# Optimization experiments

Hardware: AMD Instinct MI355X
Metric: run time of the kernel (lower is better)

The kernel has to match this reference:

```python
import jax, jax.numpy as jnp
import numpy as np

EMBED_DIM = 2048
NUM_HEADS = 16
HEAD_DIM = EMBED_DIM // NUM_HEADS
SEQ_LEN = 2048
ROPE_BASE = 10000.0


def rope_cache(seq_len, dim, base=ROPE_BASE):
    inv_freq = 1.0 / (base ** (jnp.arange(0, dim, 2, dtype=jnp.float32) / dim))
    t = jnp.arange(seq_len, dtype=jnp.float32)
    freqs = jnp.einsum('s,d->sd', t, inv_freq)  # [S, D/2]
    return jnp.cos(freqs), jnp.sin(freqs)


def apply_rope_interleaved(x, cos, sin):
    # x: [B, S, H, D]; interleaved pairs (even, odd)
    B, S, H, D = x.shape
    xp = x.reshape(B, S, H, D // 2, 2)
    x1, x2 = xp[..., 0], xp[..., 1]
    c = cos[None, :, None, :]
    s = sin[None, :, None, :]
    o1 = x1 * c - x2 * s
    o2 = x1 * s + x2 * c
    return jnp.stack([o1, o2], axis=-1).reshape(B, S, H, D)


def setup_inputs() -> dict:
    key = jax.random.key(0)
    ks = jax.random.split(key, 5)
    B = 2
    scale = 0.02
    x = jax.random.normal(ks[0], (B, SEQ_LEN, EMBED_DIM), dtype=jnp.float32)
    Wq = jax.random.normal(ks[1], (EMBED_DIM, EMBED_DIM), dtype=jnp.float32) * scale
    Wk = jax.random.normal(ks[2], (EMBED_DIM, EMBED_DIM), dtype=jnp.float32) * scale
    Wv = jax.random.normal(ks[3], (EMBED_DIM, EMBED_DIM), dtype=jnp.float32) * scale
    Wo = jax.random.normal(ks[4], (EMBED_DIM, EMBED_DIM), dtype=jnp.float32) * scale
    return {"x": x, "Wq": Wq, "Wk": Wk, "Wv": Wv, "Wo": Wo}


def reference(x, Wq, Wk, Wv, Wo):
    B, S, E = x.shape
    H, D = NUM_HEADS, HEAD_DIM
    # projections (nn.Linear: y = x @ W.T; here W stored as [out, in])
    q = (x @ Wq.T).reshape(B, S, H, D)
    k = (x @ Wk.T).reshape(B, S, H, D)
    v = (x @ Wv.T).reshape(B, S, H, D)
    cos, sin = rope_cache(S, D)
    q = apply_rope_interleaved(q, cos, sin)
    k = apply_rope_interleaved(k, cos, sin)
    # causal attention, flash-attn semantics: scale = head_dim**-0.5, fp32 softmax
    scale = 1.0 / jnp.sqrt(jnp.float32(D))
    scores = jnp.einsum('bqhd,bkhd->bhqk', q, k) * scale
    causal = jnp.tril(jnp.ones((S, S), dtype=bool))
    scores = jnp.where(causal[None, None], scores, jnp.float32(-jnp.inf))
    probs = jax.nn.softmax(scores.astype(jnp.float32), axis=-1)
    attn = jnp.einsum('bhqk,bkhd->bqhd', probs.astype(v.dtype), v)
    attn = attn.reshape(B, S, H * D)
    return attn @ Wo.T
```

## Files before the change

kernel.cpp:

```cpp
#include <hip/hip_runtime.h>
#include <cstdint>
#include <cmath>

typedef short s16x8 __attribute__((ext_vector_type(8)));
typedef float f32x4 __attribute__((ext_vector_type(4)));
typedef int   i32x4 __attribute__((ext_vector_type(4)));
typedef unsigned short u16;

#define E_DIM 2048
#define SEQ   2048
#define NB    2
#define NH    16
#define HD    128
#define BS_TOT 4096

__device__ __forceinline__ u16 f2bf(float f) {
  unsigned u = __float_as_uint(f);
  u += 0x7fffu + ((u >> 16) & 1u);
  return (u16)(u >> 16);
}
__device__ __forceinline__ float bf2f(u16 h) {
  return __uint_as_float(((unsigned)h) << 16);
}
__device__ __forceinline__ float rmax16(float v) {
  v = fmaxf(v, __shfl_xor(v, 1));
  v = fmaxf(v, __shfl_xor(v, 2));
  v = fmaxf(v, __shfl_xor(v, 4));
  v = fmaxf(v, __shfl_xor(v, 8));
  return v;
}
__device__ __forceinline__ float rsum16(float v) {
  v += __shfl_xor(v, 1);
  v += __shfl_xor(v, 2);
  v += __shfl_xor(v, 4);
  v += __shfl_xor(v, 8);
  return v;
}

__device__ __forceinline__ void gll16(const u16* g, u16* l) {
  __builtin_amdgcn_global_load_lds(
      (const __attribute__((address_space(1))) void*)g,
      (__attribute__((address_space(3))) void*)l, 16, 0, 0);
}

__global__ __launch_bounds__(256) void cast_kernel(const float* __restrict__ in,
                                                   u16* __restrict__ out) {
  const size_t t = (size_t)blockIdx.x * 256 + threadIdx.x;
  const float* p = in + t * 8;
  f32x4 a = *(const f32x4*)p;
  f32x4 b = *(const f32x4*)(p + 4);
  union { u16 u[8]; i32x4 v; } r;
  r.u[0] = f2bf(a[0]); r.u[1] = f2bf(a[1]); r.u[2] = f2bf(a[2]); r.u[3] = f2bf(a[3]);
  r.u[4] = f2bf(b[0]); r.u[5] = f2bf(b[1]); r.u[6] = f2bf(b[2]); r.u[7] = f2bf(b[3]);
  *(i32x4*)(out + t * 8) = r.v;
}

template <typename OT, bool CVTA>
__global__ __launch_bounds__(256) void gemm_nt(const void* __restrict__ Av,
                                               const u16* __restrict__ B,
                                               OT* __restrict__ C,
                                               int M, int N, int K) {
  __shared__ __align__(16) u16 As[128 * 64];
  __shared__ __align__(16) u16 Bs[128 * 64];
  const int t  = threadIdx.x;
  const int w  = t >> 6, l = t & 63, lq = l >> 4, lm = l & 15;
  const int wr = w >> 1, wc = w & 1;
  const int m0 = blockIdx.y * 128, n0 = blockIdx.x * 128;

  const f32x4 fzero = {0.f, 0.f, 0.f, 0.f};
  f32x4 acc[4][4];
#pragma unroll
  for (int mi = 0; mi < 4; ++mi)
#pragma unroll
    for (int ni = 0; ni < 4; ++ni) acc[mi][ni] = fzero;

  for (int k0 = 0; k0 < K; k0 += 64) {
    __syncthreads();
    if constexpr (CVTA) {
      const float* A = (const float*)Av;
#pragma unroll
      for (int i = 0; i < 4; ++i) {
        const int ci = i * 256 + t;
        const int r = ci >> 3, c = ci & 7, gq = c ^ (r & 7);
        const float* s = A + (size_t)(m0 + r) * K + k0 + gq * 8;
        f32x4 a = *(const f32x4*)s;
        f32x4 b = *(const f32x4*)(s + 4);
        union { u16 u[8]; i32x4 v; } rr;
        rr.u[0] = f2bf(a[0]); rr.u[1] = f2bf(a[1]); rr.u[2] = f2bf(a[2]); rr.u[3] = f2bf(a[3]);
        rr.u[4] = f2bf(b[0]); rr.u[5] = f2bf(b[1]); rr.u[6] = f2bf(b[2]); rr.u[7] = f2bf(b[3]);
        *(i32x4*)(As + ci * 8) = rr.v;
      }
    } else {
      const u16* A = (const u16*)Av;
#pragma unroll
      for (int i = 0; i < 4; ++i) {
        const int ci = i * 256 + t;
        const int r = ci >> 3, c = ci & 7, gq = c ^ (r & 7);
        gll16(A + (size_t)(m0 + r) * K + k0 + gq * 8, As + ci * 8);
      }
    }
#pragma unroll
    for (int i = 0; i < 4; ++i) {
      const int ci = i * 256 + t;
      const int r = ci >> 3, c = ci & 7, gq = c ^ (r & 7);
      gll16(B + (size_t)(n0 + r) * K + k0 + gq * 8, Bs + ci * 8);
    }
    __syncthreads();
#pragma unroll
    for (int ks = 0; ks < 2; ++ks) {
      s16x8 af[4], bf[4];
#pragma unroll
      for (int mi = 0; mi < 4; ++mi) {
        const int ra = wr * 64 + mi * 16 + lm;
        af[mi] = *(const s16x8*)(As + ra * 64 + (((ks * 4 + lq) ^ (ra & 7)) << 3));
      }
#pragma unroll
      for (int ni = 0; ni < 4; ++ni) {
        const int rb = wc * 64 + ni * 16 + lm;
        bf[ni] = *(const s16x8*)(Bs + rb * 64 + (((ks * 4 + lq) ^ (rb & 7)) << 3));
      }
#pragma unroll
      for (int mi = 0; mi < 4; ++mi)
#pragma unroll
        for (int ni = 0; ni < 4; ++ni)
          acc[mi][ni] = __builtin_amdgcn_mfma_f32_16x16x32_bf16(af[mi], bf[ni], acc[mi][ni], 0, 0, 0);
    }
  }

#pragma unroll
  for (int mi = 0; mi < 4; ++mi)
#pragma unroll
    for (int ni = 0; ni < 4; ++ni)
#pragma unroll
      for (int rr = 0; rr < 4; ++rr) {
        const int row = m0 + wr * 64 + mi * 16 + lq * 4 + rr;
        const int col = n0 + wc * 64 + ni * 16 + lm;
        const float v = acc[mi][ni][rr];
        if constexpr (sizeof(OT) == 2) {
          C[(size_t)row * N + col] = (OT)f2bf(v);
        } else {
          C[(size_t)row * N + col] = v;
        }
      }
}

__global__ __launch_bounds__(256) void gemm_qk(const u16* __restrict__ A,
                                               const u16* __restrict__ B0,
                                               const u16* __restrict__ B1,
                                               u16* __restrict__ C0,
                                               u16* __restrict__ C1) {
  constexpr int K = 2048, N = 2048;
  __shared__ __align__(16) u16 As[128 * 64];
  __shared__ __align__(16) u16 Bs[128 * 64];
  const int bx = blockIdx.x;
  const u16* B = (bx >> 4) ? B1 : B0;
  u16* C = (bx >> 4) ? C1 : C0;
  const int n0 = (bx & 15) * 128, m0 = blockIdx.y * 128;
  const int t  = threadIdx.x;
  const int w  = t >> 6, l = t & 63, lq = l >> 4, lm = l & 15;
  const int wr = w >> 1, wc = w & 1;

  const f32x4 fzero = {0.f, 0.f, 0.f, 0.f};
  f32x4 acc[4][4];
#pragma unroll
  for (int mi = 0; mi < 4; ++mi)
#pragma unroll
    for (int ni = 0; ni < 4; ++ni) acc[mi][ni] = fzero;

  for (int k0 = 0; k0 < K; k0 += 64) {
    __syncthreads();
#pragma unroll
    for (int i = 0; i < 4; ++i) {
      const int ci = i * 256 + t;
      const int r = ci >> 3, c = ci & 7, gq = c ^ (r & 7);
      gll16(A + (size_t)(m0 + r) * K + k0 + gq * 8, As + ci * 8);
    }
#pragma unroll
    for (int i = 0; i < 4; ++i) {
      const int ci = i * 256 + t;
      const int r = ci >> 3, c = ci & 7, gq = c ^ (r & 7);
      gll16(B + (size_t)(n0 + r) * K + k0 + gq * 8, Bs + ci * 8);
    }
    __syncthreads();
#pragma unroll
    for (int ks = 0; ks < 2; ++ks) {
      s16x8 af[4], bf[4];
#pragma unroll
      for (int mi = 0; mi < 4; ++mi) {
        const int ra = wr * 64 + mi * 16 + lm;
        af[mi] = *(const s16x8*)(As + ra * 64 + (((ks * 4 + lq) ^ (ra & 7)) << 3));
      }
#pragma unroll
      for (int ni = 0; ni < 4; ++ni) {
        const int rb = wc * 64 + ni * 16 + lm;
        bf[ni] = *(const s16x8*)(Bs + rb * 64 + (((ks * 4 + lq) ^ (rb & 7)) << 3));
      }
#pragma unroll
      for (int mi = 0; mi < 4; ++mi)
#pragma unroll
        for (int ni = 0; ni < 4; ++ni)
          acc[mi][ni] = __builtin_amdgcn_mfma_f32_16x16x32_bf16(af[mi], bf[ni], acc[mi][ni], 0, 0, 0);
    }
  }

#pragma unroll
  for (int mi = 0; mi < 4; ++mi)
#pragma unroll
    for (int ni = 0; ni < 4; ++ni)
#pragma unroll
      for (int rr = 0; rr < 4; ++rr) {
        const int row = m0 + wr * 64 + mi * 16 + lq * 4 + rr;
        const int col = n0 + wc * 64 + ni * 16 + lm;
        C[(size_t)row * N + col] = f2bf(acc[mi][ni][rr]);
      }
}

__global__ __launch_bounds__(256) void rope_kernel(u16* __restrict__ q, u16* __restrict__ k) {
  const float QS = 0.08838834764831845f * 1.4426950408889634f;
  const size_t t = (size_t)blockIdx.x * 256 + threadIdx.x;
  const size_t e8 = t * 8;
  const int col = (int)(e8 & (E_DIM - 1));
  const int row = (int)(e8 >> 11);
  const int s   = row & (SEQ - 1);
  const int d   = col & (HD - 1);
  float cs[4], sn[4];
#pragma unroll
  for (int j = 0; j < 4; ++j) {
    const float inv = exp2f(-0.20762050593046014f * (float)((d >> 1) + j));
    const float ang = (float)s * inv;
    sincosf(ang, &sn[j], &cs[j]);
  }
  u16* qp = q + e8;
  u16* kp = k + e8;
  union { u16 u[8]; i32x4 v; } a, b;
  a.v = *(const i32x4*)qp;
  b.v = *(const i32x4*)kp;
#pragma unroll
  for (int j = 0; j < 4; ++j) {
    const float csq = cs[j] * QS, snq = sn[j] * QS;
    const float q1 = bf2f(a.u[2 * j]), q2 = bf2f(a.u[2 * j + 1]);
    const float k1 = bf2f(b.u[2 * j]), k2 = bf2f(b.u[2 * j + 1]);
    a.u[2 * j]     = f2bf(q1 * csq - q2 * snq);
    a.u[2 * j + 1] = f2bf(q1 * snq + q2 * csq);
    b.u[2 * j]     = f2bf(k1 * cs[j] - k2 * sn[j]);
    b.u[2 * j + 1] = f2bf(k1 * sn[j] + k2 * cs[j]);
  }
  *(i32x4*)qp = a.v;
  *(i32x4*)kp = b.v;
}

__global__ __launch_bounds__(256, 2) void flash_kernel(const u16* __restrict__ q,
                                                       const u16* __restrict__ kmat,
                                                       const u16* __restrict__ vt,
                                                       u16* __restrict__ attn) {
  __shared__ __align__(16) u16 KV[32768];
  const int bx = blockIdx.x;
  const int j = bx & 15, h = (bx >> 4) & 15, b = bx >> 8;
  const int t = threadIdx.x, w = t >> 6, l = t & 63, lq = l >> 4, lm = l & 15;

  u16* myP = KV + w * 2048;
  const u16* kbase = kmat + (size_t)(b * SEQ) * E_DIM + h * HD;
  const u16* vbase = vt + (size_t)(h * HD) * BS_TOT + (size_t)b * SEQ;
  const f32x4 fzero = {0.f, 0.f, 0.f, 0.f};

  for (int pass = 0; pass < 2; ++pass) {
    const int qt = pass ? j : (31 - j);
    const int q0 = qt * 64;
    const int nT = (qt >> 1) + 1;

    const u16* qp = q + (size_t)(b * SEQ + q0 + w * 16) * E_DIM + h * HD;
    s16x8 qf[4];
#pragma unroll
    for (int kx = 0; kx < 4; ++kx)
      qf[kx] = *(const s16x8*)(qp + (size_t)lm * E_DIM + kx * 32 + lq * 8);

    float m_i[4], l_i[4];
    f32x4 acc_o[8];
#pragma unroll
    for (int rr = 0; rr < 4; ++rr) { m_i[rr] = -1e30f; l_i[rr] = 0.f; }
#pragma unroll
    for (int nd = 0; nd < 8; ++nd) acc_o[nd] = fzero;

    for (int it = 0; it < nT; ++it) {
      const int k0 = it * 128;
      __syncthreads();
#pragma unroll
      for (int i = 0; i < 8; ++i) {
        const int ci = i * 256 + t;
        const int r = ci >> 4, gq = (ci & 15) ^ (r & 15);
        gll16(kbase + (size_t)(k0 + r) * E_DIM + gq * 8, KV + ci * 8);
      }
#pragma unroll
      for (int i = 0; i < 8; ++i) {
        const int ci = i * 256 + t;
        const int r = ci >> 4, gq = (ci & 15) ^ (r & 15);
        gll16(vbase + (size_t)r * BS_TOT + k0 + gq * 8, KV + 16384 + ci * 8);
      }
      __syncthreads();

      f32x4 sc[8];
#pragma unroll
      for (int ni = 0; ni < 8; ++ni) sc[ni] = fzero;
#pragma unroll
      for (int kx = 0; kx < 4; ++kx) {
        s16x8 kf[8];
#pragma unroll
        for (int ni = 0; ni < 8; ++ni) {
          const int rn = ni * 16 + lm;
          kf[ni] = *(const s16x8*)(KV + rn * 128 + (((kx * 4 + lq) ^ lm) << 3));
        }
#pragma unroll
        for (int ni = 0; ni < 8; ++ni)
          sc[ni] = __builtin_amdgcn_mfma_f32_16x16x32_bf16(qf[kx], kf[ni], sc[ni], 0, 0, 0);
      }

      const bool diag = (it == nT - 1);
#pragma unroll
      for (int rr = 0; rr < 4; ++rr) {
        const int qrow = q0 + w * 16 + lq * 4 + rr;
        float mt = -1e30f;
#pragma unroll
        for (int ni = 0; ni < 8; ++ni) {
          float s = sc[ni][rr];
          if (diag && (k0 + ni * 16 + lm) > qrow) s = -1e30f;
          sc[ni][rr] = s;
          mt = fmaxf(mt, s);
        }
        mt = rmax16(mt);
        const float mn = fmaxf(m_i[rr], mt);
        const float al = exp2f(m_i[rr] - mn);
        float rs = 0.f;
#pragma unroll
        for (int ni = 0; ni < 8; ++ni) {
          const float p = exp2f(sc[ni][rr] - mn);
          sc[ni][rr] = p;
          rs += p;
        }
        rs = rsum16(rs);
        l_i[rr] = l_i[rr] * al + rs;
        m_i[rr] = mn;
#pragma unroll
        for (int nd = 0; nd < 8; ++nd) acc_o[nd][rr] *= al;
      }

      __syncthreads();
#pragma unroll
      for (int rr = 0; rr < 4; ++rr) {
        const int r = lq * 4 + rr;
#pragma unroll
        for (int ni = 0; ni < 8; ++ni) {
          const int c = ni * 16 + lm;
          myP[r * 128 + (((c >> 3) ^ r) << 3) + (c & 7)] = f2bf(sc[ni][rr]);
        }
      }

#pragma unroll
      for (int kx = 0; kx < 4; ++kx) {
        const s16x8 pf = *(const s16x8*)(myP + lm * 128 + (((kx * 4 + lq) ^ lm) << 3));
#pragma unroll
        for (int nd = 0; nd < 8; ++nd) {
          const int rn = nd * 16 + lm;
          const s16x8 vf = *(const s16x8*)(KV + 16384 + rn * 128 + (((kx * 4 + lq) ^ lm) << 3));
          acc_o[nd] = __builtin_amdgcn_mfma_f32_16x16x32_bf16(pf, vf, acc_o[nd], 0, 0, 0);
        }
      }
    }

    u16* op = attn + (size_t)(b * SEQ + q0 + w * 16) * E_DIM + h * HD;
#pragma unroll
    for (int rr = 0; rr < 4; ++rr) {
      const float inv = 1.0f / l_i[rr];
      const int row = lq * 4 + rr;
#pragma unroll
      for (int nd = 0; nd < 8; ++nd) {
        const int colc = nd * 16 + lm;
        op[(size_t)row * E_DIM + colc] = f2bf(acc_o[nd][rr] * inv);
      }
    }
  }
}

extern "C" void kernel_launch(void* const* d_in, const int* in_sizes, int n_in,
                              void* d_out, int out_size, void* d_ws, size_t ws_size,
                              hipStream_t stream) {
  const float* x  = (const float*)d_in[0];
  const float* Wq = (const float*)d_in[1];
  const float* Wk = (const float*)d_in[2];
  const float* Wv = (const float*)d_in[3];
  const float* Wo = (const float*)d_in[4];
  float* out = (float*)d_out;
  char* ws = (char*)d_ws;

  u16* xb    = (u16*)(ws);
  u16* vslot = (u16*)(ws + (size_t)16 * 1048576);
  u16* wq_bf = vslot;
  u16* wk_bf = vslot + (size_t)4 * 1048576;
  u16* vtb   = vslot;
  u16* wo_bf = vslot;
  u16* qb    = (u16*)d_out;
  u16* kb    = (u16*)d_out + (size_t)8 * 1048576;
  u16* attnb = xb;

  (void)in_sizes; (void)n_in; (void)out_size; (void)ws_size;

  cast_kernel<<<4096, 256, 0, stream>>>(x, xb);
  cast_kernel<<<2048, 256, 0, stream>>>(Wq, wq_bf);
  cast_kernel<<<2048, 256, 0, stream>>>(Wk, wk_bf);
  gemm_qk<<<dim3(32, 32), 256, 0, stream>>>(xb, wq_bf, wk_bf, qb, kb);
  gemm_nt<u16, true><<<dim3(32, 16), 256, 0, stream>>>(Wv, xb, vtb, 2048, 4096, 2048);
  rope_kernel<<<4096, 256, 0, stream>>>(qb, kb);
  flash_kernel<<<512, 256, 0, stream>>>(qb, kb, vtb, attnb);
  cast_kernel<<<2048, 256, 0, stream>>>(Wo, wo_bf);
  gemm_nt<float, false><<<dim3(16, 32), 256, 0, stream>>>(attnb, wo_bf, out, 4096, 2048, 2048);
}
```

Baseline: 443.9 us.

## Switch projection GEMMs to 32x32x16 MFMA and merge Wq/Wk casts

The QK, V and output projection GEMMs move from 16x16x32 MFMA tiles (4x4 per wave) to 32x32x16 MFMA tiles (2x2 per wave). This halves the LDS fragment loads per k-step and gives larger MFMA ops with better throughput per issue. The epilogue is rewritten for the 32x32 accumulator layout. Separately, the Wq and Wk fp32-to-bf16 casts are merged into a single launch to save one kernel launch.

```diff
diff --git a/kernel.cpp b/kernel.cpp
--- a/kernel.cpp
+++ b/kernel.cpp
@@ -4,6 +4,7 @@
 
 typedef short s16x8 __attribute__((ext_vector_type(8)));
 typedef float f32x4 __attribute__((ext_vector_type(4)));
+typedef float f32x16 __attribute__((ext_vector_type(16)));
 typedef int   i32x4 __attribute__((ext_vector_type(4)));
 typedef unsigned short u16;
 
@@ -55,6 +56,24 @@
   *(i32x4*)(out + t * 8) = r.v;
 }
 
+__global__ __launch_bounds__(256) void cast2_kernel(const float* __restrict__ in0,
+                                                    u16* __restrict__ out0,
+                                                    const float* __restrict__ in1,
+                                                    u16* __restrict__ out1,
+                                                    int half) {
+  const int bsel = blockIdx.x >= half;
+  const float* in = bsel ? in1 : in0;
+  u16* out = bsel ? out1 : out0;
+  const size_t t = (size_t)(blockIdx.x - (bsel ? half : 0)) * 256 + threadIdx.x;
+  const float* p = in + t * 8;
+  f32x4 a = *(const f32x4*)p;
+  f32x4 b = *(const f32x4*)(p + 4);
+  union { u16 u[8]; i32x4 v; } r;
+  r.u[0] = f2bf(a[0]); r.u[1] = f2bf(a[1]); r.u[2] = f2bf(a[2]); r.u[3] = f2bf(a[3]);
+  r.u[4] = f2bf(b[0]); r.u[5] = f2bf(b[1]); r.u[6] = f2bf(b[2]); r.u[7] = f2bf(b[3]);
+  *(i32x4*)(out + t * 8) = r.v;
+}
+
 template <typename OT, bool CVTA>
 __global__ __launch_bounds__(256) void gemm_nt(const void* __restrict__ Av,
                                                const u16* __restrict__ B,
@@ -63,16 +82,18 @@
   __shared__ __align__(16) u16 As[128 * 64];
   __shared__ __align__(16) u16 Bs[128 * 64];
   const int t  = threadIdx.x;
-  const int w  = t >> 6, l = t & 63, lq = l >> 4, lm = l & 15;
+  const int w  = t >> 6, l = t & 63;
+  const int l31 = l & 31, lh = l >> 5;
   const int wr = w >> 1, wc = w & 1;
   const int m0 = blockIdx.y * 128, n0 = blockIdx.x * 128;
 
-  const f32x4 fzero = {0.f, 0.f, 0.f, 0.f};
-  f32x4 acc[4][4];
-#pragma unroll
-  for (int mi = 0; mi < 4; ++mi)
-#pragma unroll
-    for (int ni = 0; ni < 4; ++ni) acc[mi][ni] = fzero;
+  f32x16 acc[2][2];
+#pragma unroll
+  for (int mi = 0; mi < 2; ++mi)
+#pragma unroll
+    for (int ni = 0; ni < 2; ++ni)
+#pragma unroll
+      for (int e = 0; e < 16; ++e) acc[mi][ni][e] = 0.f;
 
   for (int k0 = 0; k0 < K; k0 += 64) {
     __syncthreads();
@@ -107,41 +128,43 @@
     }
     __syncthreads();
 #pragma unroll
-    for (int ks = 0; ks < 2; ++ks) {
-      s16x8 af[4], bf[4];
-#pragma unroll
-      for (int mi = 0; mi < 4; ++mi) {
-        const int ra = wr * 64 + mi * 16 + lm;
-        af[mi] = *(const s16x8*)(As + ra * 64 + (((ks * 4 + lq) ^ (ra & 7)) << 3));
-      }
-#pragma unroll
-      for (int ni = 0; ni < 4; ++ni) {
-        const int rb = wc * 64 + ni * 16 + lm;
-        bf[ni] = *(const s16x8*)(Bs + rb * 64 + (((ks * 4 + lq) ^ (rb & 7)) << 3));
-      }
-#pragma unroll
-      for (int mi = 0; mi < 4; ++mi)
-#pragma unroll
-        for (int ni = 0; ni < 4; ++ni)
-          acc[mi][ni] = __builtin_amdgcn_mfma_f32_16x16x32_bf16(af[mi], bf[ni], acc[mi][ni], 0, 0, 0);
+    for (int ks = 0; ks < 4; ++ks) {
+      const int chunk = ks * 2 + lh;
+      s16x8 af[2], bf[2];
+#pragma unroll
+      for (int mi = 0; mi < 2; ++mi) {
+        const int ra = wr * 64 + mi * 32 + l31;
+        af[mi] = *(const s16x8*)(As + ra * 64 + ((chunk ^ (ra & 7)) << 3));
+      }
+#pragma unroll
+      for (int ni = 0; ni < 2; ++ni) {
+        const int rb = wc * 64 + ni * 32 + l31;
+        bf[ni] = *(const s16x8*)(Bs + rb * 64 + ((chunk ^ (rb & 7)) << 3));
+      }
+#pragma unroll
+      for (int mi = 0; mi < 2; ++mi)
+#pragma unroll
+        for (int ni = 0; ni < 2; ++ni)
+          acc[mi][ni] = __builtin_amdgcn_mfma_f32_32x32x16_bf16(af[mi], bf[ni], acc[mi][ni], 0, 0, 0);
     }
   }
 
 #pragma unroll
-  for (int mi = 0; mi < 4; ++mi)
-#pragma unroll
-    for (int ni = 0; ni < 4; ++ni)
-#pragma unroll
-      for (int rr = 0; rr < 4; ++rr) {
-        const int row = m0 + wr * 64 + mi * 16 + lq * 4 + rr;
-        const int col = n0 + wc * 64 + ni * 16 + lm;
-        const float v = acc[mi][ni][rr];
+  for (int mi = 0; mi < 2; ++mi)
+#pragma unroll
+    for (int ni = 0; ni < 2; ++ni) {
+      const int col = n0 + wc * 64 + ni * 32 + l31;
+#pragma unroll
+      for (int reg = 0; reg < 16; ++reg) {
+        const int row = m0 + wr * 64 + mi * 32 + 4 * lh + (reg & 3) + 8 * (reg >> 2);
+        const float v = acc[mi][ni][reg];
         if constexpr (sizeof(OT) == 2) {
           C[(size_t)row * N + col] = (OT)f2bf(v);
         } else {
           C[(size_t)row * N + col] = v;
         }
       }
+    }
 }
 
 __global__ __launch_bounds__(256) void gemm_qk(const u16* __restrict__ A,
@@ -157,15 +180,17 @@
   u16* C = (bx >> 4) ? C1 : C0;
   const int n0 = (bx & 15) * 128, m0 = blockIdx.y * 128;
   const int t  = threadIdx.x;
-  const int w  = t >> 6, l = t & 63, lq = l >> 4, lm = l & 15;
+  const int w  = t >> 6, l = t & 63;
+  const int l31 = l & 31, lh = l >> 5;
   const int wr = w >> 1, wc = w & 1;
 
-  const f32x4 fzero = {0.f, 0.f, 0.f, 0.f};
-  f32x4 acc[4][4];
-#pragma unroll
-  for (int mi = 0; mi < 4; ++mi)
-#pragma unroll
-    for (int ni = 0; ni < 4; ++ni) acc[mi][ni] = fzero;
+  f32x16 acc[2][2];
+#pragma unroll
+  for (int mi = 0; mi < 2; ++mi)
+#pragma unroll
+    for (int ni = 0; ni < 2; ++ni)
+#pragma unroll
+      for (int e = 0; e < 16; ++e) acc[mi][ni][e] = 0.f;
 
   for (int k0 = 0; k0 < K; k0 += 64) {
     __syncthreads();
@@ -183,36 +208,38 @@
     }
     __syncthreads();
 #pragma unroll
-    for (int ks = 0; ks < 2; ++ks) {
-      s16x8 af[4], bf[4];
-#pragma unroll
-      for (int mi = 0; mi < 4; ++mi) {
-        const int ra = wr * 64 + mi * 16 + lm;
-        af[mi] = *(const s16x8*)(As + ra * 64 + (((ks * 4 + lq) ^ (ra & 7)) << 3));
-      }
-#pragma unroll
-      for (int ni = 0; ni < 4; ++ni) {
-        const int rb = wc * 64 + ni * 16 + lm;
-        bf[ni] = *(const s16x8*)(Bs + rb * 64 + (((ks * 4 + lq) ^ (rb & 7)) << 3));
-      }
-#pragma unroll
-      for (int mi = 0; mi < 4; ++mi)
-#pragma unroll
-        for (int ni = 0; ni < 4; ++ni)
-          acc[mi][ni] = __builtin_amdgcn_mfma_f32_16x16x32_bf16(af[mi], bf[ni], acc[mi][ni], 0, 0, 0);
+    for (int ks = 0; ks < 4; ++ks) {
+      const int chunk = ks * 2 + lh;
+      s16x8 af[2], bf[2];
+#pragma unroll
+      for (int mi = 0; mi < 2; ++mi) {
+        const int ra = wr * 64 + mi * 32 + l31;
+        af[mi] = *(const s16x8*)(As + ra * 64 + ((chunk ^ (ra & 7)) << 3));
+      }
+#pragma unroll
+      for (int ni = 0; ni < 2; ++ni) {
+        const int rb = wc * 64 + ni * 32 + l31;
+        bf[ni] = *(const s16x8*)(Bs + rb * 64 + ((chunk ^ (rb & 7)) << 3));
+      }
+#pragma unroll
+      for (int mi = 0; mi < 2; ++mi)
+#pragma unroll
+        for (int ni = 0; ni < 2; ++ni)
+          acc[mi][ni] = __builtin_amdgcn_mfma_f32_32x32x16_bf16(af[mi], bf[ni], acc[mi][ni], 0, 0, 0);
     }
   }
 
 #pragma unroll
-  for (int mi = 0; mi < 4; ++mi)
-#pragma unroll
-    for (int ni = 0; ni < 4; ++ni)
-#pragma unroll
-      for (int rr = 0; rr < 4; ++rr) {
-        const int row = m0 + wr * 64 + mi * 16 + lq * 4 + rr;
-        const int col = n0 + wc * 64 + ni * 16 + lm;
-        C[(size_t)row * N + col] = f2bf(acc[mi][ni][rr]);
-      }
+  for (int mi = 0; mi < 2; ++mi)
+#pragma unroll
+    for (int ni = 0; ni < 2; ++ni) {
+      const int col = n0 + wc * 64 + ni * 32 + l31;
+#pragma unroll
+      for (int reg = 0; reg < 16; ++reg) {
+        const int row = m0 + wr * 64 + mi * 32 + 4 * lh + (reg & 3) + 8 * (reg >> 2);
+        C[(size_t)row * N + col] = f2bf(acc[mi][ni][reg]);
+      }
+    }
 }
 
 __global__ __launch_bounds__(256) void rope_kernel(u16* __restrict__ q, u16* __restrict__ k) {
@@ -404,8 +431,7 @@
   (void)in_sizes; (void)n_in; (void)out_size; (void)ws_size;
 
   cast_kernel<<<4096, 256, 0, stream>>>(x, xb);
-  cast_kernel<<<2048, 256, 0, stream>>>(Wq, wq_bf);
-  cast_kernel<<<2048, 256, 0, stream>>>(Wk, wk_bf);
+  cast2_kernel<<<4096, 256, 0, stream>>>(Wq, wq_bf, Wk, wk_bf, 2048);
   gemm_qk<<<dim3(32, 32), 256, 0, stream>>>(xb, wq_bf, wk_bf, qb, kb);
   gemm_nt<u16, true><<<dim3(32, 16), 256, 0, stream>>>(Wv, xb, vtb, 2048, 4096, 2048);
   rope_kernel<<<4096, 256, 0, stream>>>(qb, kb);
```

Result: no change. 440.2 us (-0.8%).
